# Kernel optimization log

Hardware: AMD Instinct MI355X
Metric: run time of the kernel (lower is better)

## Reference

```python
import jax, jax.numpy as jnp
import numpy as np

D_MODEL = 1024
N_HEADS = 16
D_HEAD = D_MODEL // N_HEADS
B, T = 2, 2048


def setup_inputs() -> dict:
    key = jax.random.key(0)
    k1, k2, k3 = jax.random.split(key, 3)
    x = jax.random.normal(k1, (B, T, D_MODEL), dtype=jnp.float32)
    # torch nn.Linear weights: y = x @ W.T, W has shape [out, in]
    W_qkv = jax.random.normal(k2, (3 * D_MODEL, D_MODEL), dtype=jnp.float32) * (1.0 / np.sqrt(D_MODEL))
    W_out = jax.random.normal(k3, (D_MODEL, D_MODEL), dtype=jnp.float32) * (1.0 / np.sqrt(D_MODEL))
    return {"x": x, "W_qkv": W_qkv, "W_out": W_out}


def reference(x, W_qkv, W_out):
    Bb, Tt, Dd = x.shape
    qkv = (x @ W_qkv.T).reshape(Bb, Tt, 3, N_HEADS, D_HEAD)
    q, k, v = qkv[:, :, 0], qkv[:, :, 1], qkv[:, :, 2]  # [B,T,H,d]
    q = q.transpose(0, 2, 1, 3)  # [B,H,T,d]
    k = k.transpose(0, 2, 1, 3)
    v = v.transpose(0, 2, 1, 3)
    scale = 1.0 / np.sqrt(D_HEAD)
    scores = jnp.einsum('bhqd,bhkd->bhqk', q, k) * scale  # [B,H,T,T]
    causal = jnp.tril(jnp.ones((Tt, Tt), dtype=bool))
    scores = jnp.where(causal, scores, -jnp.inf)
    A = jax.nn.softmax(scores, axis=-1)
    AV = jnp.einsum('bhqk,bhkd->bhqd', A, v)
    AAV = jnp.einsum('bhqk,bhkd->bhqd', A, AV)  # twicing correction
    out = 2.0 * AV - AAV  # [B,H,T,d]
    out = out.transpose(0, 2, 1, 3).reshape(Bb, Tt, Dd)
    return out @ W_out.T
```

## Files before the change

### kernel.cpp

```cpp
#include <hip/hip_runtime.h>
#include <hip/hip_bf16.h>

#define T_SEQ  2048
#define DMODEL 1024
#define NH     16
#define DH     64
#define NTOK   4096
#define QSCALE 0.18033688011112042f
#define M_FIX  16.0f

typedef unsigned short u16;
typedef short s16x8 __attribute__((ext_vector_type(8)));
typedef unsigned short u16x8 __attribute__((ext_vector_type(8)));
typedef float f32x4 __attribute__((ext_vector_type(4)));

__device__ __forceinline__ u16 f2bf(float f) {
  unsigned u = __float_as_uint(f);
  u += 0x7FFFu + ((u >> 16) & 1u);
  return (u16)(u >> 16);
}
__device__ __forceinline__ unsigned pk2(float a, float b) {
  __hip_bfloat162 h = __float22bfloat162_rn(make_float2(a, b));
  unsigned u;
  __builtin_memcpy(&u, &h, 4);
  return u;
}
__device__ __forceinline__ unsigned pk2z(float a, float b) {
  return __builtin_amdgcn_perm(__float_as_uint(b), __float_as_uint(a), 0x07060302);
}
__device__ __forceinline__ float bf2f(u16 x) {
  return __uint_as_float(((unsigned)x) << 16);
}
__device__ __forceinline__ void async_cp16(const u16* g, u16* l) {
  __builtin_amdgcn_global_load_lds(
      (const __attribute__((address_space(1))) unsigned*)g,
      (__attribute__((address_space(3))) unsigned*)l, 16, 0, 0);
}

__global__ void cast_to_bf16(const float* __restrict__ in, u16* __restrict__ out, int n4) {
  int i = blockIdx.x * blockDim.x + threadIdx.x;
  if (i >= n4) return;
  float4 v = reinterpret_cast<const float4*>(in)[i];
  ushort4 r;
  r.x = f2bf(v.x); r.y = f2bf(v.y); r.z = f2bf(v.z); r.w = f2bf(v.w);
  reinterpret_cast<ushort4*>(out)[i] = r;
}

template <int EPI>
__global__ __launch_bounds__(256) void gemm128(
    const u16* __restrict__ A, const u16* __restrict__ Bm,
    int M, int N, int K,
    u16* __restrict__ outQ, u16* __restrict__ outK,
    u16* __restrict__ outT, float* __restrict__ outF) {
  __shared__ __align__(16) u16 SM[16384];
  const int tid = threadIdx.x, wave = tid >> 6, lane = tid & 63;
  const int f15 = lane & 15, quad = lane >> 4;
  const int bm = blockIdx.x * 128, bn = blockIdx.y * 128;
  const int wr = wave >> 1, wc = wave & 1;

  f32x4 acc[4][4] = {};

  const u16* Ag0 = A  + (size_t)(bm + (2 * wave) * 16 + f15) * K + quad * 8;
  const u16* Ag1 = A  + (size_t)(bm + (2 * wave + 1) * 16 + f15) * K + quad * 8;
  const u16* Bg0 = Bm + (size_t)(bn + (2 * wave) * 16 + f15) * K + quad * 8;
  const u16* Bg1 = Bm + (size_t)(bn + (2 * wave + 1) * 16 + f15) * K + quad * 8;
  u16* LA0 = SM + (2 * wave) * 512 + lane * 8;
  u16* LA1 = SM + (2 * wave + 1) * 512 + lane * 8;
  u16* LB0 = SM + 4096 + (2 * wave) * 512 + lane * 8;
  u16* LB1 = SM + 4096 + (2 * wave + 1) * 512 + lane * 8;

  const int KT = K >> 5;
  async_cp16(Ag0, LA0); async_cp16(Ag1, LA1);
  async_cp16(Bg0, LB0); async_cp16(Bg1, LB1);
  __syncthreads();

  for (int kt = 0; kt < KT; kt++) {
    const int buf = kt & 1;
    if (kt + 1 < KT) {
      const int k0 = (kt + 1) * 32;
      const int o = (buf ^ 1) * 8192;
      async_cp16(Ag0 + k0, LA0 + o); async_cp16(Ag1 + k0, LA1 + o);
      async_cp16(Bg0 + k0, LB0 + o); async_cp16(Bg1 + k0, LB1 + o);
    }
    const u16* Af = SM + buf * 8192;
    const u16* Bf = SM + buf * 8192 + 4096;
    s16x8 af[4], bfr[4];
#pragma unroll
    for (int mi = 0; mi < 4; mi++)
      af[mi] = *reinterpret_cast<const s16x8*>(Af + (wr * 4 + mi) * 512 + lane * 8);
#pragma unroll
    for (int ni = 0; ni < 4; ni++)
      bfr[ni] = *reinterpret_cast<const s16x8*>(Bf + (wc * 4 + ni) * 512 + lane * 8);
#pragma unroll
    for (int mi = 0; mi < 4; mi++)
#pragma unroll
      for (int ni = 0; ni < 4; ni++)
        acc[mi][ni] = __builtin_amdgcn_mfma_f32_16x16x32_bf16(af[mi], bfr[ni], acc[mi][ni], 0, 0, 0);
    __syncthreads();
  }

  if (EPI == 2) {
#pragma unroll
    for (int mi = 0; mi < 4; mi++)
#pragma unroll
      for (int ni = 0; ni < 4; ni++)
#pragma unroll
        for (int r = 0; r < 4; r++)
          outF[(size_t)(bm + wr * 64 + mi * 16 + quad * 4 + r) * N + bn + wc * 64 + ni * 16 + f15] =
              acc[mi][ni][r];
    return;
  }
  const float scale = (EPI == 0 && bn < 1024) ? QSCALE : 1.0f;
  u16* Cs = SM;
#pragma unroll
  for (int h2 = 0; h2 < 2; h2++) {
    __syncthreads();
    if (wr == h2) {
#pragma unroll
      for (int mi = 0; mi < 4; mi++)
#pragma unroll
        for (int ni = 0; ni < 4; ni++) {
          int c = wc * 64 + ni * 16 + f15;
          int cp;
          if (EPI == 1) {
            int cc = c & 63;
            cp = (c & 64) + (cc >> 5) * 32 + ((cc >> 2) & 3) * 8 + ((cc >> 4) & 1) * 4 + (cc & 3);
          } else cp = c;
#pragma unroll
          for (int r = 0; r < 4; r++)
            Cs[(mi * 16 + quad * 4 + r) * 136 + cp] = f2bf(acc[mi][ni][r] * scale);
        }
    }
    __syncthreads();
    const int row = tid >> 2, cs = (tid & 3) * 32;
    const int gm = bm + h2 * 64 + row;
#pragma unroll
    for (int c8 = 0; c8 < 4; c8++) {
      int gc = bn + cs + c8 * 8;
      u16x8 v = *reinterpret_cast<const u16x8*>(&Cs[row * 136 + cs + c8 * 8]);
      if (EPI == 0) {
        int which = gc >> 10, hh = (gc >> 6) & 15, d = gc & 63;
        u16* dst = (which ? outK : outQ) + ((size_t)hh * NTOK + gm) * 64 + d;
        *reinterpret_cast<u16x8*>(dst) = v;
      } else {
        *reinterpret_cast<u16x8*>(outT + (size_t)gm * N + gc) = v;
      }
    }
  }
}

template <int PASS>
__global__ __launch_bounds__(256) void attn_pass(
    const u16* __restrict__ Qb, const u16* __restrict__ Kb, const u16* __restrict__ Vsrc,
    float* __restrict__ LinvG, u16* __restrict__ Vp2, u16* __restrict__ TW) {
  __shared__ __align__(16) u16 SM[16384];
  const int tid = threadIdx.x, wave = tid >> 6, lane = tid & 63;
  const int f15 = lane & 15, quad = lane >> 4;
  const int bid = blockIdx.x;
  const int y = (bid & 7) * 4 + ((bid >> 3) & 3);
  const int b = y >> 4, h = y & 15;
  const int g = bid >> 5, a = g & 7;
  const int gq = g >> 3;
  const int qt = (gq == 0) ? (31 - a) : (gq == 1) ? (8 + a) : (gq == 2) ? (23 - a) : a;
  const int q0 = qt * 64;
  const int ntiles = qt + 1;
  const size_t qk_base = ((size_t)h * NTOK + (size_t)b * T_SEQ) * 64;
  const size_t vt_base = (size_t)h * 64 * NTOK + (size_t)b * T_SEQ;

  const int qw = q0 + 16 * wave;
  s16x8 qf0, qf1;
  {
    const u16* qp = Qb + qk_base + (size_t)(qw + f15) * 64 + quad * 8;
    qf0 = *reinterpret_cast<const s16x8*>(qp);
    qf1 = *reinterpret_cast<const s16x8*>(qp + 32);
  }
  float invl_r = 0.f;
  if (PASS == 1) invl_r = LinvG[(size_t)y * T_SEQ + qw + f15];

  f32x4 accO[4] = {};
  float l_acc = 0.f;

  const u16* Kg = Kb  + qk_base + (size_t)(wave * 16 + f15) * 64 + quad * 8;
  const u16* Vg = Vsrc + vt_base + (size_t)(wave * 16 + f15) * NTOK + quad * 8;
  u16* LK = SM + (wave * 2) * 512 + lane * 8;
  u16* LV = SM + 4096 + (wave * 2) * 512 + lane * 8;

  async_cp16(Kg, LK); async_cp16(Kg + 32, LK + 512);
  async_cp16(Vg, LV); async_cp16(Vg + 32, LV + 512);
  __syncthreads();

  for (int ti = 0; ti < ntiles; ti++) {
    const int buf = ti & 1;
    if (ti + 1 < ntiles) {
      const int j1 = (ti + 1) * 64;
      const int o = (buf ^ 1) * 8192;
      async_cp16(Kg + (size_t)j1 * 64, LK + o);
      async_cp16(Kg + (size_t)j1 * 64 + 32, LK + o + 512);
      async_cp16(Vg + j1, LV + o);
      async_cp16(Vg + j1 + 32, LV + o + 512);
    }
    const u16* Kf = SM + buf * 8192;
    const u16* Vf = SM + buf * 8192 + 4096;

    f32x4 accS[4] = {};
#pragma unroll
    for (int st = 0; st < 4; st++) {
      s16x8 k0 = *reinterpret_cast<const s16x8*>(Kf + (st * 2) * 512 + lane * 8);
      s16x8 k1 = *reinterpret_cast<const s16x8*>(Kf + (st * 2 + 1) * 512 + lane * 8);
      accS[st] = __builtin_amdgcn_mfma_f32_16x16x32_bf16(k0, qf0, accS[st], 0, 0, 0);
      accS[st] = __builtin_amdgcn_mfma_f32_16x16x32_bf16(k1, qf1, accS[st], 0, 0, 0);
    }
    union pbu { s16x8 v; unsigned u[4]; } pb0, pb1;
    if (ti < qt) {
#pragma unroll
      for (int st = 0; st < 4; st++) {
        float e0 = __builtin_amdgcn_exp2f(accS[st][0] - M_FIX);
        float e1 = __builtin_amdgcn_exp2f(accS[st][1] - M_FIX);
        float e2 = __builtin_amdgcn_exp2f(accS[st][2] - M_FIX);
        float e3 = __builtin_amdgcn_exp2f(accS[st][3] - M_FIX);
        if (PASS == 0) l_acc += (e0 + e1) + (e2 + e3);
        unsigned w0 = pk2z(e0, e1), w1 = pk2z(e2, e3);
        if (st < 2) { pb0.u[(st & 1) * 2] = w0; pb0.u[(st & 1) * 2 + 1] = w1; }
        else        { pb1.u[(st & 1) * 2] = w0; pb1.u[(st & 1) * 2 + 1] = w1; }
      }
    } else {
      const int qrel = 16 * wave + f15;
#pragma unroll
      for (int st = 0; st < 4; st++) {
        const int jb = st * 16 + quad * 4;
        float e0 = (jb + 0 <= qrel) ? __builtin_amdgcn_exp2f(accS[st][0] - M_FIX) : 0.f;
        float e1 = (jb + 1 <= qrel) ? __builtin_amdgcn_exp2f(accS[st][1] - M_FIX) : 0.f;
        float e2 = (jb + 2 <= qrel) ? __builtin_amdgcn_exp2f(accS[st][2] - M_FIX) : 0.f;
        float e3 = (jb + 3 <= qrel) ? __builtin_amdgcn_exp2f(accS[st][3] - M_FIX) : 0.f;
        if (PASS == 0) l_acc += (e0 + e1) + (e2 + e3);
        unsigned w0 = pk2z(e0, e1), w1 = pk2z(e2, e3);
        if (st < 2) { pb0.u[(st & 1) * 2] = w0; pb0.u[(st & 1) * 2 + 1] = w1; }
        else        { pb1.u[(st & 1) * 2] = w0; pb1.u[(st & 1) * 2 + 1] = w1; }
      }
    }
#pragma unroll
    for (int mt = 0; mt < 4; mt++) {
      s16x8 v0 = *reinterpret_cast<const s16x8*>(Vf + (mt * 2) * 512 + lane * 8);
      s16x8 v1 = *reinterpret_cast<const s16x8*>(Vf + (mt * 2 + 1) * 512 + lane * 8);
      accO[mt] = __builtin_amdgcn_mfma_f32_16x16x32_bf16(v0, pb0.v, accO[mt], 0, 0, 0);
      accO[mt] = __builtin_amdgcn_mfma_f32_16x16x32_bf16(v1, pb1.v, accO[mt], 0, 0, 0);
    }
    __syncthreads();
  }

  if (PASS == 0) {
    float l = l_acc;
    l += __shfl_xor(l, 16);
    l += __shfl_xor(l, 32);
    invl_r = 1.0f / l;
    if (quad == 0) LinvG[(size_t)y * T_SEQ + qw + f15] = invl_r;
  }

  if (PASS == 0) {
    u16* E = SM;
    const int ql = 16 * wave + f15;
    const int slot = (ql >> 5) * 32 + ((ql >> 2) & 3) * 8 + ((ql >> 4) & 1) * 4 + (ql & 3);
#pragma unroll
    for (int mt = 0; mt < 4; mt++)
#pragma unroll
      for (int r = 0; r < 4; r++)
        E[(mt * 16 + quad * 4 + r) * 68 + slot] = f2bf(accO[mt][r] * invl_r);
    __syncthreads();
    const int d = tid >> 2, s = (tid & 3) * 16;
    const u16* vg2 = Vsrc + vt_base + (size_t)d * NTOK + q0 + s;
    u16* og = Vp2 + vt_base + (size_t)d * NTOK + q0 + s;
#pragma unroll
    for (int g2 = 0; g2 < 2; g2++) {
      u16x8 vv = *reinterpret_cast<const u16x8*>(vg2 + g2 * 8);
      u16x8 ee = *reinterpret_cast<const u16x8*>(&E[d * 68 + s + g2 * 8]);
      u16x8 oo;
#pragma unroll
      for (int i = 0; i < 8; i++) oo[i] = f2bf(2.0f * bf2f(vv[i]) - bf2f(ee[i]));
      *reinterpret_cast<u16x8*>(og + g2 * 8) = oo;
    }
  } else {
    u16* E2 = SM;
#pragma unroll
    for (int mt = 0; mt < 4; mt++) {
      uint2 w;
      w.x = pk2(accO[mt][0] * invl_r, accO[mt][1] * invl_r);
      w.y = pk2(accO[mt][2] * invl_r, accO[mt][3] * invl_r);
      *reinterpret_cast<uint2*>(&E2[(16 * wave + f15) * 72 + mt * 16 + quad * 4]) = w;
    }
    __syncthreads();
    const int q = tid >> 2, s = (tid & 3) * 16;
    u16* dst = TW + ((size_t)b * T_SEQ + q0 + q) * DMODEL + h * 64 + s;
    *reinterpret_cast<u16x8*>(dst) = *reinterpret_cast<const u16x8*>(&E2[q * 72 + s]);
    *reinterpret_cast<u16x8*>(dst + 8) = *reinterpret_cast<const u16x8*>(&E2[q * 72 + s + 8]);
  }
}

extern "C" void kernel_launch(void* const* d_in, const int* in_sizes, int n_in,
                              void* d_out, int out_size, void* d_ws, size_t ws_size,
                              hipStream_t stream) {
  const float* x    = (const float*)d_in[0];
  const float* Wqkv = (const float*)d_in[1];
  const float* Wout = (const float*)d_in[2];
  float* out = (float*)d_out;
  char* ws = (char*)d_ws;

  u16*   Xb    = (u16*)(ws + 0);
  u16*   Wqkvb = (u16*)(ws + 8388608);
  u16*   Woutb = (u16*)(ws + 14680064);
  u16*   Qb    = (u16*)(ws + 16777216);
  u16*   Kb    = (u16*)(ws + 25165824);
  u16*   Vtp   = (u16*)(ws + 33554432);
  u16*   TW    = (u16*)(ws + 41943040);
  u16*   Vp2   = (u16*)(ws + 50331648);
  float* LinvG = (float*)(ws + 58720256);

  cast_to_bf16<<<4096, 256, 0, stream>>>(x, Xb, 1048576);
  cast_to_bf16<<<3072, 256, 0, stream>>>(Wqkv, Wqkvb, 786432);
  cast_to_bf16<<<1024, 256, 0, stream>>>(Wout, Woutb, 262144);

  gemm128<0><<<dim3(32, 16), 256, 0, stream>>>(Xb, Wqkvb, NTOK, 2048, DMODEL,
                                               Qb, Kb, nullptr, nullptr);
  gemm128<1><<<dim3(8, 32), 256, 0, stream>>>(Wqkvb + 2048 * 1024, Xb, 1024, NTOK, DMODEL,
                                              nullptr, nullptr, Vtp, nullptr);

  attn_pass<0><<<1024, 256, 0, stream>>>(Qb, Kb, Vtp, LinvG, Vp2, nullptr);
  attn_pass<1><<<1024, 256, 0, stream>>>(Qb, Kb, Vp2, LinvG, nullptr, TW);

  gemm128<2><<<dim3(32, 8), 256, 0, stream>>>(TW, Woutb, NTOK, DMODEL, DMODEL,
                                              nullptr, nullptr, nullptr, out);
}
```

Baseline: 247.1 us.

## Fuse QKV projection GEMMs into one launch and retile output GEMM

```diff
diff --git a/kernel.cpp b/kernel.cpp
--- a/kernel.cpp
+++ b/kernel.cpp
@@ -46,17 +46,15 @@
   reinterpret_cast<ushort4*>(out)[i] = r;
 }
 
-template <int EPI>
-__global__ __launch_bounds__(256) void gemm128(
+__global__ __launch_bounds__(256) void gemm_qkv(
     const u16* __restrict__ A, const u16* __restrict__ Bm,
-    int M, int N, int K,
-    u16* __restrict__ outQ, u16* __restrict__ outK,
-    u16* __restrict__ outT, float* __restrict__ outF) {
+    u16* __restrict__ outQ, u16* __restrict__ outK, u16* __restrict__ outV) {
   __shared__ __align__(16) u16 SM[16384];
   const int tid = threadIdx.x, wave = tid >> 6, lane = tid & 63;
   const int f15 = lane & 15, quad = lane >> 4;
   const int bm = blockIdx.x * 128, bn = blockIdx.y * 128;
   const int wr = wave >> 1, wc = wave & 1;
+  const int K = DMODEL;
 
   f32x4 acc[4][4] = {};
 
@@ -99,54 +97,123 @@
     __syncthreads();
   }
 
-  if (EPI == 2) {
-#pragma unroll
-    for (int mi = 0; mi < 4; mi++)
-#pragma unroll
-      for (int ni = 0; ni < 4; ni++)
-#pragma unroll
-        for (int r = 0; r < 4; r++)
-          outF[(size_t)(bm + wr * 64 + mi * 16 + quad * 4 + r) * N + bn + wc * 64 + ni * 16 + f15] =
-              acc[mi][ni][r];
-    return;
-  }
-  const float scale = (EPI == 0 && bn < 1024) ? QSCALE : 1.0f;
   u16* Cs = SM;
-#pragma unroll
-  for (int h2 = 0; h2 < 2; h2++) {
-    __syncthreads();
-    if (wr == h2) {
-#pragma unroll
-      for (int mi = 0; mi < 4; mi++)
-#pragma unroll
-        for (int ni = 0; ni < 4; ni++) {
-          int c = wc * 64 + ni * 16 + f15;
-          int cp;
-          if (EPI == 1) {
-            int cc = c & 63;
-            cp = (c & 64) + (cc >> 5) * 32 + ((cc >> 2) & 3) * 8 + ((cc >> 4) & 1) * 4 + (cc & 3);
-          } else cp = c;
-#pragma unroll
-          for (int r = 0; r < 4; r++)
-            Cs[(mi * 16 + quad * 4 + r) * 136 + cp] = f2bf(acc[mi][ni][r] * scale);
-        }
-    }
-    __syncthreads();
-    const int row = tid >> 2, cs = (tid & 3) * 32;
-    const int gm = bm + h2 * 64 + row;
-#pragma unroll
-    for (int c8 = 0; c8 < 4; c8++) {
-      int gc = bn + cs + c8 * 8;
-      u16x8 v = *reinterpret_cast<const u16x8*>(&Cs[row * 136 + cs + c8 * 8]);
-      if (EPI == 0) {
+  if (bn < 2048) {
+    const float scale = (bn < 1024) ? QSCALE : 1.0f;
+#pragma unroll
+    for (int h2 = 0; h2 < 2; h2++) {
+      __syncthreads();
+      if (wr == h2) {
+#pragma unroll
+        for (int mi = 0; mi < 4; mi++)
+#pragma unroll
+          for (int ni = 0; ni < 4; ni++) {
+            int c = wc * 64 + ni * 16 + f15;
+#pragma unroll
+            for (int r = 0; r < 4; r++)
+              Cs[(mi * 16 + quad * 4 + r) * 136 + c] = f2bf(acc[mi][ni][r] * scale);
+          }
+      }
+      __syncthreads();
+      const int row = tid >> 2, cs = (tid & 3) * 32;
+      const int gm = bm + h2 * 64 + row;
+#pragma unroll
+      for (int c8 = 0; c8 < 4; c8++) {
+        int gc = bn + cs + c8 * 8;
+        u16x8 v = *reinterpret_cast<const u16x8*>(&Cs[row * 136 + cs + c8 * 8]);
         int which = gc >> 10, hh = (gc >> 6) & 15, d = gc & 63;
         u16* dst = (which ? outK : outQ) + ((size_t)hh * NTOK + gm) * 64 + d;
         *reinterpret_cast<u16x8*>(dst) = v;
-      } else {
-        *reinterpret_cast<u16x8*>(outT + (size_t)gm * N + gc) = v;
-      }
-    }
-  }
+      }
+    }
+  } else {
+    const int bnV = bn - 2048;
+#pragma unroll
+    for (int h2 = 0; h2 < 2; h2++) {
+      __syncthreads();
+      if (wr == h2) {
+#pragma unroll
+        for (int mi = 0; mi < 4; mi++)
+#pragma unroll
+          for (int ni = 0; ni < 4; ni++) {
+            int c = wc * 64 + ni * 16 + f15;
+#pragma unroll
+            for (int r = 0; r < 4; r++)
+              Cs[(mi * 16 + quad * 4 + r) * 138 + c] = f2bf(acc[mi][ni][r]);
+          }
+      }
+      __syncthreads();
+      const int fd = tid >> 3, s8 = (tid & 7) * 8;
+      const int tb = ((s8 >> 5) & 1) * 32 + ((s8 >> 3) & 3) * 4;
+      const int gmb = bm + h2 * 64;
+#pragma unroll
+      for (int p = 0; p < 4; p++) {
+        const int d = p * 32 + fd;
+        u16x8 vv;
+#pragma unroll
+        for (int j = 0; j < 4; j++) vv[j] = Cs[(tb + j) * 138 + d];
+#pragma unroll
+        for (int j = 0; j < 4; j++) vv[4 + j] = Cs[(tb + 16 + j) * 138 + d];
+        *reinterpret_cast<u16x8*>(outV + (size_t)(bnV + d) * NTOK + gmb + s8) = vv;
+      }
+    }
+  }
+}
+
+__global__ __launch_bounds__(256) void gemm_out(
+    const u16* __restrict__ A, const u16* __restrict__ Bm, float* __restrict__ outF) {
+  __shared__ __align__(16) u16 SM[12288];
+  const int tid = threadIdx.x, wave = tid >> 6, lane = tid & 63;
+  const int f15 = lane & 15, quad = lane >> 4;
+  const int bm = blockIdx.x * 64, bn = blockIdx.y * 128;
+  const int wr = wave >> 1, wc = wave & 1;
+  const int K = DMODEL, N = DMODEL;
+
+  f32x4 acc[2][4] = {};
+
+  const u16* Ag = A  + (size_t)(bm + wave * 16 + f15) * K + quad * 8;
+  const u16* Bg0 = Bm + (size_t)(bn + (2 * wave) * 16 + f15) * K + quad * 8;
+  const u16* Bg1 = Bm + (size_t)(bn + (2 * wave + 1) * 16 + f15) * K + quad * 8;
+  u16* LA  = SM + wave * 512 + lane * 8;
+  u16* LB0 = SM + 2048 + (2 * wave) * 512 + lane * 8;
+  u16* LB1 = SM + 2048 + (2 * wave + 1) * 512 + lane * 8;
+
+  const int KT = K >> 5;
+  async_cp16(Ag, LA); async_cp16(Bg0, LB0); async_cp16(Bg1, LB1);
+  __syncthreads();
+
+  for (int kt = 0; kt < KT; kt++) {
+    const int buf = kt & 1;
+    if (kt + 1 < KT) {
+      const int k0 = (kt + 1) * 32;
+      const int o = (buf ^ 1) * 6144;
+      async_cp16(Ag + k0, LA + o); async_cp16(Bg0 + k0, LB0 + o); async_cp16(Bg1 + k0, LB1 + o);
+    }
+    const u16* Af = SM + buf * 6144;
+    const u16* Bf = SM + buf * 6144 + 2048;
+    s16x8 af[2], bfr[4];
+#pragma unroll
+    for (int mi = 0; mi < 2; mi++)
+      af[mi] = *reinterpret_cast<const s16x8*>(Af + (wr * 2 + mi) * 512 + lane * 8);
+#pragma unroll
+    for (int ni = 0; ni < 4; ni++)
+      bfr[ni] = *reinterpret_cast<const s16x8*>(Bf + (wc * 4 + ni) * 512 + lane * 8);
+#pragma unroll
+    for (int mi = 0; mi < 2; mi++)
+#pragma unroll
+      for (int ni = 0; ni < 4; ni++)
+        acc[mi][ni] = __builtin_amdgcn_mfma_f32_16x16x32_bf16(af[mi], bfr[ni], acc[mi][ni], 0, 0, 0);
+    __syncthreads();
+  }
+
+#pragma unroll
+  for (int mi = 0; mi < 2; mi++)
+#pragma unroll
+    for (int ni = 0; ni < 4; ni++)
+#pragma unroll
+      for (int r = 0; r < 4; r++)
+        outF[(size_t)(bm + wr * 32 + mi * 16 + quad * 4 + r) * N + bn + wc * 64 + ni * 16 + f15] =
+            acc[mi][ni][r];
 }
 
 template <int PASS>
@@ -318,14 +385,10 @@
   cast_to_bf16<<<3072, 256, 0, stream>>>(Wqkv, Wqkvb, 786432);
   cast_to_bf16<<<1024, 256, 0, stream>>>(Wout, Woutb, 262144);
 
-  gemm128<0><<<dim3(32, 16), 256, 0, stream>>>(Xb, Wqkvb, NTOK, 2048, DMODEL,
-                                               Qb, Kb, nullptr, nullptr);
-  gemm128<1><<<dim3(8, 32), 256, 0, stream>>>(Wqkvb + 2048 * 1024, Xb, 1024, NTOK, DMODEL,
-                                              nullptr, nullptr, Vtp, nullptr);
+  gemm_qkv<<<dim3(32, 24), 256, 0, stream>>>(Xb, Wqkvb, Qb, Kb, Vtp);
 
   attn_pass<0><<<1024, 256, 0, stream>>>(Qb, Kb, Vtp, LinvG, Vp2, nullptr);
   attn_pass<1><<<1024, 256, 0, stream>>>(Qb, Kb, Vp2, LinvG, nullptr, TW);
 
-  gemm128<2><<<dim3(32, 8), 256, 0, stream>>>(TW, Woutb, NTOK, DMODEL, DMODEL,
-                                              nullptr, nullptr, nullptr, out);
-}
+  gemm_out<<<dim3(64, 8), 256, 0, stream>>>(TW, Woutb, out);
+}
```

Result: no change. 243.4 us (-1.5%).
